# Performance work log

Hardware: AMD Instinct MI355X
Metric: run time of the kernel (lower is better)

The kernel has to match this reference:

```python
import jax, jax.numpy as jnp
import numpy as np

T, B, IN, H, O = 512, 128, 128, 512, 64
ALPHA_NOISE = 0.2      # OU noise time constant
ALPHA_NEURON = 0.1     # neuron leak
NOISE_SD = 0.5         # rnn noise std
W_SCALE = 0.05         # keep pre-sigmoid activations in a sane range


def setup_inputs() -> dict:
    key = jax.random.key(0)
    ks = jax.random.split(key, 12)
    f32 = jnp.float32
    return {
        "x1": jax.random.normal(ks[0], (T, B, IN), f32),
        "x2": jax.random.normal(ks[1], (T, B, IN), f32),
        "eps1": jax.random.normal(ks[2], (T, B, H), f32),
        "eps2": jax.random.normal(ks[3], (T, B, H), f32),
        "w_in1": jax.random.normal(ks[4], (IN, H), f32) * W_SCALE,
        "w_in2": jax.random.normal(ks[5], (IN, H), f32) * W_SCALE,
        "w_rnn11": jax.random.normal(ks[6], (H, H), f32) * W_SCALE,
        "w_rnn12": jax.random.normal(ks[7], (H, H), f32) * W_SCALE,
        "w_rnn21": jax.random.normal(ks[8], (H, H), f32) * W_SCALE,
        "w_rnn22": jax.random.normal(ks[9], (H, H), f32) * W_SCALE,
        "w_out_dm": jax.random.normal(ks[10], (H, O), f32) * W_SCALE,
        "w_out_em": jax.random.normal(ks[11], (H, O), f32) * W_SCALE,
    }


def reference(x1, x2, eps1, eps2, w_in1, w_in2, w_rnn11, w_rnn12,
              w_rnn21, w_rnn22, w_out_dm, w_out_em):
    decay = jnp.exp(jnp.asarray(-ALPHA_NOISE, x1.dtype))
    nscale = jnp.sqrt(1.0 - jnp.exp(jnp.asarray(-2.0 * ALPHA_NOISE, x1.dtype))) * NOISE_SD
    an = jnp.asarray(ALPHA_NEURON, x1.dtype)

    def step(carry, xs):
        n1, n2, h1, h2 = carry
        x1t, x2t, e1, e2 = xs
        # OU noise update
        n1 = n1 * decay + nscale * e1
        n2 = n2 * decay + nscale * e2
        # population 1 updates first; population 2 sees the NEW h1 (as in torch code)
        h1 = h1 * (1.0 - an) + an * jax.nn.sigmoid(
            x1t @ w_in1 + h1 @ w_rnn11 + h2 @ w_rnn21 + n1)
        h2 = h2 * (1.0 - an) + an * jax.nn.sigmoid(
            x2t @ w_in2 + h1 @ w_rnn12 + h2 @ w_rnn22 + n2)
        return (n1, n2, h1, h2), (h1, h2)

    z = jnp.zeros((x1.shape[1], w_rnn11.shape[0]), x1.dtype)  # [B,H]
    (_, _, _, _), (h1s, h2s) = jax.lax.scan(step, (z, z, z, z), (x1, x2, eps1, eps2))
    hsum = h1s + h2s                         # [T,B,H]
    y_dm = jnp.einsum('tbh,ho->tbo', hsum, w_out_dm)
    y_em = jnp.einsum('tbh,ho->tbo', hsum, w_out_em)
    return y_dm, y_em
```

## Files before the change

### kernel.cpp

```cpp
#include <hip/hip_runtime.h>
#include <cstdint>
#include <cstddef>

#define TT 512
#define BB 128
#define IN_DIM 128
#define HH 512
#define OO 64

#define DECAY  0.8187307530779818f
#define NSCALE 0.2870887f

typedef unsigned short u16;
typedef float f32x4 __attribute__((ext_vector_type(4)));
typedef short bf8 __attribute__((ext_vector_type(8)));

__device__ __forceinline__ u16 f2bf(float f) {
  union { float f; uint32_t u; } v; v.f = f;
  uint32_t r = v.u + 0x7FFFu + ((v.u >> 16) & 1u);
  return (u16)(r >> 16);
}

__device__ __forceinline__ f32x4 mfma16(bf8 a, bf8 b, f32x4 c) {
  return __builtin_amdgcn_mfma_f32_16x16x32_bf16(a, b, c, 0, 0, 0);
}

__global__ void wprep_kernel(
    const float* __restrict__ win1, const float* __restrict__ win2,
    const float* __restrict__ w11,  const float* __restrict__ w12,
    const float* __restrict__ w21,  const float* __restrict__ w22,
    const float* __restrict__ wdm,  const float* __restrict__ wem,
    u16* __restrict__ waf, u16* __restrict__ wbf, u16* __restrict__ wof) {
  size_t idx = (size_t)blockIdx.x * 256 + threadIdx.x;
  const size_t NWA = 32u * 36u * 512u;
  if (idx < 2 * NWA) {
    int isB = idx >= NWA;
    size_t i = isB ? (idx - NWA) : idx;
    int js  = (int)(i / (36 * 512));
    int rem = (int)(i % (36 * 512));
    int kb  = rem / 512;
    int li  = rem % 512;
    int lane = li >> 3, e = li & 7;
    int j    = js * 16 + (lane & 15);
    int koff = ((lane >> 4) << 3) + e;
    float val;
    if (kb < 4) {
      int k = kb * 32 + koff;
      val = (isB ? win2 : win1)[(size_t)k * HH + j];
    } else if (kb < 20) {
      int k = (kb - 4) * 32 + koff;
      val = (isB ? w12 : w11)[(size_t)k * HH + j];
    } else {
      int k = (kb - 20) * 32 + koff;
      val = (isB ? w22 : w21)[(size_t)k * HH + j];
    }
    (isB ? wbf : waf)[i] = f2bf(val);
  } else if (idx < 2 * NWA + 8u * 16u * 512u) {
    size_t i = idx - 2 * NWA;
    int js  = (int)(i / (16 * 512));
    int rem = (int)(i % (16 * 512));
    int kb  = rem / 512;
    int li  = rem % 512;
    int lane = li >> 3, e = li & 7;
    int j = js * 16 + (lane & 15);
    int k = kb * 32 + ((lane >> 4) << 3) + e;
    float val = (j < 64) ? wdm[(size_t)k * OO + j] : wem[(size_t)k * OO + (j - 64)];
    wof[i] = f2bf(val);
  }
}

__global__ __launch_bounds__(128) void step_kernel(
    const u16* a_h1, const u16* a_h2, u16* hc_out,
    const float* __restrict__ x,
    const float* __restrict__ eps,
    const u16* __restrict__ wf,
    float* __restrict__ hf,
    float* __restrict__ nf,
    const float* __restrict__ h_other,
    u16* __restrict__ hsum_t,
    int t, int dst_off) {
  int js = blockIdx.x & 31;
  int mg = blockIdx.x >> 5;
  int tid = threadIdx.x;
  int w = tid >> 6;
  int l = tid & 63;
  int jc = js * 16;
  int rowbase = mg * 32 + w * 16;

  __shared__ u16 wlds[36 * 512];
  {
    const uint32_t* src = (const uint32_t*)(wf + (size_t)js * (36 * 512));
    uint32_t* dst = (uint32_t*)wlds;
#pragma unroll
    for (int i = 0; i < 72; ++i) dst[tid + i * 128] = src[tid + i * 128];
  }
  __syncthreads();

  int arow = rowbase + (l & 15);
  int kgrp = (l >> 4) * 8;

  f32x4 acc = {0.f, 0.f, 0.f, 0.f};

  const float* xrow = x + ((size_t)t * BB + arow) * IN_DIM;
#pragma unroll
  for (int kb = 0; kb < 4; ++kb) {
    const float* xp = xrow + kb * 32 + kgrp;
    bf8 af;
#pragma unroll
    for (int e = 0; e < 8; ++e) af[e] = (short)f2bf(xp[e]);
    bf8 bfr = *(const bf8*)(wlds + kb * 512 + l * 8);
    acc = mfma16(af, bfr, acc);
  }
  {
    const u16* h1row = a_h1 + (size_t)arow * 1024;
#pragma unroll
    for (int kb = 4; kb < 20; ++kb) {
      bf8 af = *(const bf8*)(h1row + (kb - 4) * 32 + kgrp);
      bf8 bfr = *(const bf8*)(wlds + kb * 512 + l * 8);
      acc = mfma16(af, bfr, acc);
    }
  }
  {
    const u16* h2row = a_h2 + (size_t)arow * 1024 + 512;
#pragma unroll
    for (int kb = 20; kb < 36; ++kb) {
      bf8 af = *(const bf8*)(h2row + (kb - 20) * 32 + kgrp);
      bf8 bfr = *(const bf8*)(wlds + kb * 512 + l * 8);
      acc = mfma16(af, bfr, acc);
    }
  }

  int colg = jc + (l & 15);
  int row0 = rowbase + ((l >> 4) << 2);
#pragma unroll
  for (int r = 0; r < 4; ++r) {
    int row = row0 + r;
    size_t off = (size_t)row * HH + colg;
    float e = eps[((size_t)t * BB + row) * HH + colg];
    float n = nf[off] * DECAY + NSCALE * e;
    float pre = acc[r] + n;
    float s = 1.0f / (1.0f + __expf(-pre));
    float h = hf[off] * 0.9f + 0.1f * s;
    nf[off] = n;
    hf[off] = h;
    hc_out[(size_t)row * 1024 + dst_off + colg] = f2bf(h);
    if (hsum_t) hsum_t[off] = f2bf(h_other[off] + h);
  }
}

__global__ __launch_bounds__(256) void outgemm_kernel(
    const u16* __restrict__ hs, const u16* __restrict__ wof,
    float* __restrict__ out) {
  int ng = blockIdx.x & 3;
  int mg = blockIdx.x >> 2;
  int tid = threadIdx.x;
  int w = tid >> 6, l = tid & 63;

  __shared__ u16 wlds[2 * 16 * 512];
  {
    const uint32_t* src = (const uint32_t*)(wof + (size_t)ng * (2 * 16 * 512));
    uint32_t* dst = (uint32_t*)wlds;
#pragma unroll
    for (int i = 0; i < 32; ++i) dst[tid + i * 256] = src[tid + i * 256];
  }
  __syncthreads();

  int mbase = mg * 64 + w * 16;
  int arow = mbase + (l & 15);
  int kgrp = (l >> 4) * 8;
  const u16* ap = hs + (size_t)arow * HH;

  f32x4 acc0 = {0.f, 0.f, 0.f, 0.f}, acc1 = {0.f, 0.f, 0.f, 0.f};
#pragma unroll
  for (int kb = 0; kb < 16; ++kb) {
    bf8 a = *(const bf8*)(ap + kb * 32 + kgrp);
    bf8 b0 = *(const bf8*)(wlds + kb * 512 + l * 8);
    bf8 b1 = *(const bf8*)(wlds + 8192 + kb * 512 + l * 8);
    acc0 = mfma16(a, b0, acc0);
    acc1 = mfma16(a, b1, acc1);
  }

  int row0 = mbase + ((l >> 4) << 2);
  float* out_em = out + (size_t)TT * BB * OO;
#pragma unroll
  for (int q = 0; q < 2; ++q) {
    f32x4 acc = q ? acc1 : acc0;
    int jg = ng * 32 + q * 16 + (l & 15);
    float* base = (jg < 64) ? out : out_em;
    int col = jg & 63;
#pragma unroll
    for (int r = 0; r < 4; ++r)
      base[(size_t)(row0 + r) * OO + col] = acc[r];
  }
}

extern "C" void kernel_launch(void* const* d_in, const int* in_sizes, int n_in,
                              void* d_out, int out_size, void* d_ws, size_t ws_size,
                              hipStream_t stream) {
  const float* x1   = (const float*)d_in[0];
  const float* x2   = (const float*)d_in[1];
  const float* eps1 = (const float*)d_in[2];
  const float* eps2 = (const float*)d_in[3];
  const float* win1 = (const float*)d_in[4];
  const float* win2 = (const float*)d_in[5];
  const float* w11  = (const float*)d_in[6];
  const float* w12  = (const float*)d_in[7];
  const float* w21  = (const float*)d_in[8];
  const float* w22  = (const float*)d_in[9];
  const float* wdm  = (const float*)d_in[10];
  const float* wem  = (const float*)d_in[11];

  char* ws = (char*)d_ws;
  u16*   HC  = (u16*)(ws + 0);
  float* H1F = (float*)(ws + 524288);
  float* H2F = (float*)(ws + 786432);
  float* N1F = (float*)(ws + 1048576);
  float* N2F = (float*)(ws + 1310720);
  u16*   WAF = (u16*)(ws + 1572864);
  u16*   WBF = (u16*)(ws + 2752512);
  u16*   WOF = (u16*)(ws + 3932160);
  u16*   HS  = (u16*)(ws + 4194304);

  hipMemsetAsync(ws, 0, 1572864, stream);

  wprep_kernel<<<4864, 256, 0, stream>>>(win1, win2, w11, w12, w21, w22,
                                         wdm, wem, WAF, WBF, WOF);

  for (int t = 0; t < TT; ++t) {
    u16* hin  = HC + (size_t)(t & 1) * 131072;
    u16* hout = HC + (size_t)((t + 1) & 1) * 131072;
    step_kernel<<<128, 128, 0, stream>>>(hin, hin, hout, x1, eps1, WAF,
                                         H1F, N1F, nullptr, nullptr, t, 0);
    step_kernel<<<128, 128, 0, stream>>>(hout, hin, hout, x2, eps2, WBF,
                                         H2F, N2F, H1F,
                                         HS + (size_t)t * BB * HH, t, 512);
  }

  outgemm_kernel<<<4096, 256, 0, stream>>>(HS, WOF, (float*)d_out);
}
```

Measured before the change: 8.800 ms.

## Replace per-step kernel launches with persistent scan kernel using flag-based sync

Measured after the change: 23.74 ms. 2.7x slower.

```diff
diff --git a/kernel.cpp b/kernel.cpp
--- a/kernel.cpp
+++ b/kernel.cpp
@@ -20,7 +20,10 @@
   uint32_t r = v.u + 0x7FFFu + ((v.u >> 16) & 1u);
   return (u16)(r >> 16);
 }
-
+__device__ __forceinline__ float bf2f(u16 u) {
+  union { uint32_t u; float f; } v; v.u = (uint32_t)u << 16;
+  return v.f;
+}
 __device__ __forceinline__ f32x4 mfma16(bf8 a, bf8 b, f32x4 c) {
   return __builtin_amdgcn_mfma_f32_16x16x32_bf16(a, b, c, 0, 0, 0);
 }
@@ -69,82 +72,115 @@
   }
 }
 
-__global__ __launch_bounds__(128) void step_kernel(
-    const u16* a_h1, const u16* a_h2, u16* hc_out,
-    const float* __restrict__ x,
-    const float* __restrict__ eps,
-    const u16* __restrict__ wf,
-    float* __restrict__ hf,
-    float* __restrict__ nf,
-    const float* __restrict__ h_other,
-    u16* __restrict__ hsum_t,
-    int t, int dst_off) {
-  int js = blockIdx.x & 31;
-  int mg = blockIdx.x >> 5;
-  int tid = threadIdx.x;
-  int w = tid >> 6;
-  int l = tid & 63;
-  int jc = js * 16;
-  int rowbase = mg * 32 + w * 16;
-
-  __shared__ u16 wlds[36 * 512];
-  {
-    const uint32_t* src = (const uint32_t*)(wf + (size_t)js * (36 * 512));
-    uint32_t* dst = (uint32_t*)wlds;
-#pragma unroll
-    for (int i = 0; i < 72; ++i) dst[tid + i * 128] = src[tid + i * 128];
-  }
-  __syncthreads();
-
-  int arow = rowbase + (l & 15);
-  int kgrp = (l >> 4) * 8;
-
-  f32x4 acc = {0.f, 0.f, 0.f, 0.f};
-
-  const float* xrow = x + ((size_t)t * BB + arow) * IN_DIM;
-#pragma unroll
-  for (int kb = 0; kb < 4; ++kb) {
-    const float* xp = xrow + kb * 32 + kgrp;
-    bf8 af;
-#pragma unroll
-    for (int e = 0; e < 8; ++e) af[e] = (short)f2bf(xp[e]);
-    bf8 bfr = *(const bf8*)(wlds + kb * 512 + l * 8);
-    acc = mfma16(af, bfr, acc);
-  }
-  {
-    const u16* h1row = a_h1 + (size_t)arow * 1024;
+__global__ __launch_bounds__(256, 1) void scan_kernel(
+    const float* __restrict__ x1,   const float* __restrict__ x2,
+    const float* __restrict__ eps1, const float* __restrict__ eps2,
+    const u16* __restrict__ waf, const u16* __restrict__ wbf,
+    u16* mir, int* flags, u16* __restrict__ hs) {
+  int g      = blockIdx.x & 7;
+  int member = blockIdx.x >> 3;
+  int wid    = member * 4 + (threadIdx.x >> 6);
+  int l      = threadIdx.x & 63;
+  int phase  = wid >> 5;
+  int nt     = wid & 31;
+
+  const u16* wbase = (phase ? wbf : waf) + (size_t)nt * (36 * 512);
+  bf8 w[36];
+#pragma unroll
+  for (int kb = 0; kb < 36; ++kb)
+    w[kb] = *(const bf8*)(wbase + kb * 512 + l * 8);
+
+  u16* gm = mir + (size_t)g * 32768;
+  int* flagA = flags + g * 32;
+  int* flagB = flagA + 1;
+
+  const float* x   = phase ? x2 : x1;
+  const float* eps = phase ? eps2 : eps1;
+
+  int al    = l & 15;
+  int kgrp  = (l >> 4) * 8;
+  int row0  = (l >> 4) * 4;
+  int colg  = nt * 16 + al;
+  int growA = g * 16 + al;
+  int growC = g * 16 + row0;
+
+  float nreg[4] = {0.f, 0.f, 0.f, 0.f};
+  float hreg[4] = {0.f, 0.f, 0.f, 0.f};
+
+  for (int t = 0; t < TT; ++t) {
+    const float* xp = x + ((size_t)t * BB + growA) * IN_DIM + kgrp;
+    bf8 xa[4];
+#pragma unroll
+    for (int kb = 0; kb < 4; ++kb) {
+      f32x4 lo = *(const f32x4*)(xp + kb * 32);
+      f32x4 hi = *(const f32x4*)(xp + kb * 32 + 4);
+      bf8 a;
+#pragma unroll
+      for (int e = 0; e < 4; ++e) {
+        a[e]     = (short)f2bf(lo[e]);
+        a[4 + e] = (short)f2bf(hi[e]);
+      }
+      xa[kb] = a;
+    }
+    float epsv[4];
+#pragma unroll
+    for (int r = 0; r < 4; ++r)
+      epsv[r] = eps[((size_t)t * BB + growC + r) * HH + colg];
+
+    {
+      int* fp  = phase ? flagA : flagB;
+      int  tgt = phase ? 32 * (t + 1) : 32 * t;
+      while (__hip_atomic_load(fp, __ATOMIC_RELAXED, __HIP_MEMORY_SCOPE_AGENT) < tgt)
+        __builtin_amdgcn_s_sleep(1);
+      __threadfence();
+    }
+
+    int p = t & 1, q = p ^ 1;
+    const u16* h1r = gm + (phase ? q : p) * 8192;
+    const u16* h2r = gm + 16384 + p * 8192;
+    u16* dst = phase ? (gm + 16384 + q * 8192) : (gm + q * 8192);
+
+    f32x4 acc[4];
+#pragma unroll
+    for (int i = 0; i < 4; ++i) acc[i] = (f32x4){0.f, 0.f, 0.f, 0.f};
+#pragma unroll
+    for (int kb = 0; kb < 4; ++kb)
+      acc[kb] = mfma16(xa[kb], w[kb], acc[kb]);
+    const u16* h1p = h1r + al * 512 + kgrp;
 #pragma unroll
     for (int kb = 4; kb < 20; ++kb) {
-      bf8 af = *(const bf8*)(h1row + (kb - 4) * 32 + kgrp);
-      bf8 bfr = *(const bf8*)(wlds + kb * 512 + l * 8);
-      acc = mfma16(af, bfr, acc);
-    }
-  }
-  {
-    const u16* h2row = a_h2 + (size_t)arow * 1024 + 512;
+      bf8 a = *(const bf8*)(h1p + (kb - 4) * 32);
+      acc[kb & 3] = mfma16(a, w[kb], acc[kb & 3]);
+    }
+    const u16* h2p = h2r + al * 512 + kgrp;
 #pragma unroll
     for (int kb = 20; kb < 36; ++kb) {
-      bf8 af = *(const bf8*)(h2row + (kb - 20) * 32 + kgrp);
-      bf8 bfr = *(const bf8*)(wlds + kb * 512 + l * 8);
-      acc = mfma16(af, bfr, acc);
-    }
-  }
-
-  int colg = jc + (l & 15);
-  int row0 = rowbase + ((l >> 4) << 2);
-#pragma unroll
-  for (int r = 0; r < 4; ++r) {
-    int row = row0 + r;
-    size_t off = (size_t)row * HH + colg;
-    float e = eps[((size_t)t * BB + row) * HH + colg];
-    float n = nf[off] * DECAY + NSCALE * e;
-    float pre = acc[r] + n;
-    float s = 1.0f / (1.0f + __expf(-pre));
-    float h = hf[off] * 0.9f + 0.1f * s;
-    nf[off] = n;
-    hf[off] = h;
-    hc_out[(size_t)row * 1024 + dst_off + colg] = f2bf(h);
-    if (hsum_t) hsum_t[off] = f2bf(h_other[off] + h);
+      bf8 a = *(const bf8*)(h2p + (kb - 20) * 32);
+      acc[kb & 3] = mfma16(a, w[kb], acc[kb & 3]);
+    }
+    f32x4 accs = (acc[0] + acc[1]) + (acc[2] + acc[3]);
+
+#pragma unroll
+    for (int r = 0; r < 4; ++r) {
+      nreg[r] = nreg[r] * DECAY + NSCALE * epsv[r];
+      float pre = accs[r] + nreg[r];
+      float s = 1.0f / (1.0f + __expf(-pre));
+      hreg[r] = hreg[r] * 0.9f + 0.1f * s;
+      dst[(row0 + r) * 512 + colg] = f2bf(hreg[r]);
+    }
+    if (phase) {
+      const u16* h1n = gm + q * 8192;
+#pragma unroll
+      for (int r = 0; r < 4; ++r) {
+        float h1v = bf2f(h1n[(row0 + r) * 512 + colg]);
+        hs[((size_t)t * BB + growC + r) * HH + colg] = f2bf(h1v + hreg[r]);
+      }
+    }
+
+    __threadfence();
+    if (l == 0)
+      __hip_atomic_fetch_add(phase ? flagB : flagA, 1,
+                             __ATOMIC_RELEASE, __HIP_MEMORY_SCOPE_AGENT);
   }
 }
 
@@ -173,7 +209,7 @@
   f32x4 acc0 = {0.f, 0.f, 0.f, 0.f}, acc1 = {0.f, 0.f, 0.f, 0.f};
 #pragma unroll
   for (int kb = 0; kb < 16; ++kb) {
-    bf8 a = *(const bf8*)(ap + kb * 32 + kgrp);
+    bf8 a  = *(const bf8*)(ap + kb * 32 + kgrp);
     bf8 b0 = *(const bf8*)(wlds + kb * 512 + l * 8);
     bf8 b1 = *(const bf8*)(wlds + 8192 + kb * 512 + l * 8);
     acc0 = mfma16(a, b0, acc0);
@@ -211,30 +247,20 @@
   const float* wem  = (const float*)d_in[11];
 
   char* ws = (char*)d_ws;
-  u16*   HC  = (u16*)(ws + 0);
-  float* H1F = (float*)(ws + 524288);
-  float* H2F = (float*)(ws + 786432);
-  float* N1F = (float*)(ws + 1048576);
-  float* N2F = (float*)(ws + 1310720);
-  u16*   WAF = (u16*)(ws + 1572864);
-  u16*   WBF = (u16*)(ws + 2752512);
-  u16*   WOF = (u16*)(ws + 3932160);
-  u16*   HS  = (u16*)(ws + 4194304);
-
-  hipMemsetAsync(ws, 0, 1572864, stream);
+  u16*  MIR   = (u16*)(ws + 0);
+  int*  FLAGS = (int*)(ws + 524288);
+  u16*  WAF   = (u16*)(ws + 1048576);
+  u16*  WBF   = (u16*)(ws + 2228224);
+  u16*  WOF   = (u16*)(ws + 3407872);
+  u16*  HS    = (u16*)(ws + 4194304);
+
+  hipMemsetAsync(ws, 0, 525312, stream);
 
   wprep_kernel<<<4864, 256, 0, stream>>>(win1, win2, w11, w12, w21, w22,
                                          wdm, wem, WAF, WBF, WOF);
 
-  for (int t = 0; t < TT; ++t) {
-    u16* hin  = HC + (size_t)(t & 1) * 131072;
-    u16* hout = HC + (size_t)((t + 1) & 1) * 131072;
-    step_kernel<<<128, 128, 0, stream>>>(hin, hin, hout, x1, eps1, WAF,
-                                         H1F, N1F, nullptr, nullptr, t, 0);
-    step_kernel<<<128, 128, 0, stream>>>(hout, hin, hout, x2, eps2, WBF,
-                                         H2F, N2F, H1F,
-                                         HS + (size_t)t * BB * HH, t, 512);
-  }
+  scan_kernel<<<128, 256, 0, stream>>>(x1, x2, eps1, eps2, WAF, WBF,
+                                       MIR, FLAGS, HS);
 
   outgemm_kernel<<<4096, 256, 0, stream>>>(HS, WOF, (float*)d_out);
 }
```
